# Kernel tuning notes

Measured on AMD Instinct MI355X. Metric: run time of the kernel, lower is better.

Reference implementation:

```python
import jax, jax.numpy as jnp
import numpy as np

SCALE = 20.0
THRESHOLD = 0.9995


def setup_inputs() -> dict:
    key = jax.random.key(0)
    k1, k2, k3 = jax.random.split(key, 3)
    B, C, H, W, S = 4, 128, 96, 128, 1024
    # L2-normalize along channel so the dot product is a true cosine in [-1, 1]
    # (keeps exp(scale * (x - threshold)) numerically sane, as intended by the module).
    def unit(x):
        return x / (jnp.linalg.norm(x, axis=1, keepdims=True) + 1e-8)
    source_feature_map = unit(jax.random.normal(k1, (B, C, H, W), dtype=jnp.float32))
    target_feature_map = unit(jax.random.normal(k2, (B, C, H, W), dtype=jnp.float32))
    source_feature_1D_locations = jax.random.randint(k3, (B, S, 1), 0, H * W, dtype=jnp.int64)
    mask = jnp.ones((B, 1, H, W), dtype=jnp.float32)
    return {
        "source_feature_map": source_feature_map,
        "target_feature_map": target_feature_map,
        "source_feature_1D_locations": source_feature_1D_locations,
        "mask": mask,
    }


def reference(source_feature_map, target_feature_map, source_feature_1D_locations, mask):
    B, C, H, W = source_feature_map.shape
    loc = source_feature_1D_locations[..., 0]  # [B, S]
    src_flat = source_feature_map.reshape(B, C, H * W)  # [B, C, HW]
    # gather sampled query vectors: [B, C, S]
    sampled = jnp.take_along_axis(src_flat, loc[:, None, :], axis=2)
    # per-batch 1x1 conv == batched matmul: [B, S, H, W]
    corr = jnp.einsum('bchw,bcs->bshw', target_feature_map, sampled)
    resp = jnp.exp(SCALE * (0.5 * corr + 0.5 - THRESHOLD)) * mask  # mask broadcasts [B,1,H,W]
    resp = resp / jnp.sum(resp, axis=(2, 3), keepdims=True)
    return resp
```

## Files before the change

kernel.cpp:

```cpp
#include <hip/hip_runtime.h>

typedef unsigned int u32;
typedef unsigned short u16;
typedef short s8v __attribute__((ext_vector_type(8)));
typedef float f16v __attribute__((ext_vector_type(16)));
typedef _Float16 h8 __attribute__((ext_vector_type(8)));

#define NB 4
#define NC 128
#define HW 12288
#define NS 1024

#define EXP_A 10.0f
#define EXP_B (-9.99f)
#define ESCALE 4096.0f

#define TS 256
#define TP 256
#define NPT (HW/TP)
#define NST (NS/TS)

__device__ inline u16 f2bf(float f) {
    u32 u = __float_as_uint(f);
    return (u16)((u + 0x7fffu + ((u >> 16) & 1u)) >> 16);
}
__device__ inline float bf2f(u16 h) { return __uint_as_float(((u32)h) << 16); }

__device__ inline void gload_lds16(const void* g, void* l) {
    __builtin_amdgcn_global_load_lds(
        (const __attribute__((address_space(1))) void*)g,
        (__attribute__((address_space(3))) void*)l, 16, 0, 0);
}

__global__ __launch_bounds__(256) void prep(
    const float* __restrict__ src, const float* __restrict__ tgt,
    const int* __restrict__ loc,
    u16* __restrict__ ahi, u16* __restrict__ alo,
    u16* __restrict__ bhi, u16* __restrict__ blo,
    float* __restrict__ sums)
{
    int blk = blockIdx.x, t = threadIdx.x;
    if (blk < (HW / 64) * NB) {
        int b = blk / (HW / 64), pt = blk - b * (HW / 64);
        int pxl = t & 63, u = t >> 6;
        int px = pt * 64 + pxl;
        int slot = u ^ ((px >> 1) & 3);
#pragma unroll
        for (int kc = 0; kc < 4; ++kc) {
            int c0 = kc * 32 + u * 8;
            u32 hq[4], lq[4];
#pragma unroll
            for (int k = 0; k < 4; ++k) {
                float v0 = tgt[((size_t)(b * NC + c0 + 2 * k)) * HW + px];
                float v1 = tgt[((size_t)(b * NC + c0 + 2 * k + 1)) * HW + px];
                u16 h0 = f2bf(v0), h1 = f2bf(v1);
                u16 l0 = f2bf(v0 - bf2f(h0)), l1 = f2bf(v1 - bf2f(h1));
                hq[k] = (u32)h0 | ((u32)h1 << 16);
                lq[k] = (u32)l0 | ((u32)l1 << 16);
            }
            size_t off = (((size_t)((b * 4 + kc) * HW + px)) * 4 + slot) * 8;
            *(uint4*)(bhi + off) = make_uint4(hq[0], hq[1], hq[2], hq[3]);
            *(uint4*)(blo + off) = make_uint4(lq[0], lq[1], lq[2], lq[3]);
        }
    } else {
        int sb = blk - (HW / 64) * NB;
        int gid = sb * 256 + t;
        if (gid < NB * NS) sums[gid] = 0.0f;
        int bs = sb * 2 + (t >> 7);
        int c  = t & 127;
        int b  = bs >> 10, s = bs & 1023;
        int l  = loc[bs];
        float v = src[((size_t)(b * NC + c)) * HW + l];
        u16 h  = f2bf(v);
        u16 lo = f2bf(v - bf2f(h));
        int kc = c >> 5, u = (c >> 3) & 3, e = c & 7;
        int slot = u ^ ((s >> 1) & 3);
        size_t off = ((size_t)((b * 4 + kc) * NS + s)) * 32 + slot * 8 + e;
        ahi[off] = h;
        alo[off] = lo;
    }
}

template <int F16>
__global__ __launch_bounds__(512) void corr_fused(
    const u16* __restrict__ bhi, const u16* __restrict__ blo,
    const u16* __restrict__ ahi, const u16* __restrict__ alo,
    const float* __restrict__ mask, float* __restrict__ sums,
    _Float16* __restrict__ ebuf, float* __restrict__ out)
{
    __shared__ __align__(1024) char sm[65536];

    int f = blockIdx.x;
    int xcd = f & 7, r0 = f >> 3;
    int st = r0 & 3;
    int p  = (r0 >> 2) * 8 + xcd;
    int b  = p / 48, pt = p - b * 48;

    int t = threadIdx.x, w = t >> 6, l = t & 63, ln = l & 31, h = l >> 5;
    int ws = w >> 1, wp = w & 1;

    f16v acc[2][4];
#pragma unroll
    for (int i = 0; i < 2; ++i)
#pragma unroll
        for (int j = 0; j < 4; ++j)
#pragma unroll
            for (int r = 0; r < 16; ++r) acc[i][j][r] = 0.0f;

    for (int kc = 0; kc < 4; ++kc) {
        const char* ga_h = (const char*)ahi + ((size_t)((b * 4 + kc) * NS + st * TS)) * 64;
        const char* ga_l = (const char*)alo + ((size_t)((b * 4 + kc) * NS + st * TS)) * 64;
        const char* gb_h = (const char*)bhi + ((size_t)((b * 4 + kc) * HW + pt * TP)) * 64;
        const char* gb_l = (const char*)blo + ((size_t)((b * 4 + kc) * HW + pt * TP)) * 64;
#pragma unroll
        for (int it = 0; it < 8; ++it) {
            int q = w * 8 + it;
            int rg = q >> 4, inner = q & 15;
            const char* gb = rg == 0 ? ga_h : rg == 1 ? ga_l : rg == 2 ? gb_h : gb_l;
            gload_lds16(gb + inner * 1024 + l * 16, sm + q * 1024);
        }
        __syncthreads();

#pragma unroll
        for (int kk2 = 0; kk2 < 2; ++kk2) {
            int u = kk2 * 2 + h;
            s8v a_h[2], a_l[2], b_h[4], b_l[4];
#pragma unroll
            for (int i = 0; i < 2; ++i) {
                int row = ws * 64 + i * 32 + ln;
                int sl = u ^ ((row >> 1) & 3);
                a_h[i] = *(const s8v*)(sm + 0 * 16384 + row * 64 + sl * 16);
                a_l[i] = *(const s8v*)(sm + 1 * 16384 + row * 64 + sl * 16);
            }
#pragma unroll
            for (int j = 0; j < 4; ++j) {
                int px = wp * 128 + j * 32 + ln;
                int sl = u ^ ((px >> 1) & 3);
                b_h[j] = *(const s8v*)(sm + 2 * 16384 + px * 64 + sl * 16);
                b_l[j] = *(const s8v*)(sm + 3 * 16384 + px * 64 + sl * 16);
            }
            __builtin_amdgcn_s_setprio(1);
#pragma unroll
            for (int i = 0; i < 2; ++i)
#pragma unroll
                for (int j = 0; j < 4; ++j) {
                    acc[i][j] = __builtin_amdgcn_mfma_f32_32x32x16_bf16(a_h[i], b_h[j], acc[i][j], 0, 0, 0);
                    acc[i][j] = __builtin_amdgcn_mfma_f32_32x32x16_bf16(a_l[i], b_h[j], acc[i][j], 0, 0, 0);
                    acc[i][j] = __builtin_amdgcn_mfma_f32_32x32x16_bf16(a_h[i], b_l[j], acc[i][j], 0, 0, 0);
                }
            __builtin_amdgcn_s_setprio(0);
        }
        __syncthreads();
    }

    float mvs[4];
#pragma unroll
    for (int j = 0; j < 4; ++j)
        mvs[j] = mask[(size_t)b * HW + pt * TP + wp * 128 + j * 32 + ln] * ESCALE;

    float* rs = (float*)sm;
    size_t base = ((size_t)(b * NS + st * TS)) * HW + pt * TP + wp * 128 + ln;
    _Float16* eb0 = ebuf + base;
    float*    ob0 = out  + base;
#pragma unroll
    for (int i = 0; i < 2; ++i) {
        int rb = ws * 64 + i * 32 + 4 * h;
#pragma unroll
        for (int r = 0; r < 16; ++r) {
            int row = rb + (r & 3) + 8 * (r >> 2);
            float tot = 0.0f;
#pragma unroll
            for (int j = 0; j < 4; ++j) {
                float e = __expf(fmaf(acc[i][j][r], EXP_A, EXP_B)) * mvs[j];
                if (F16) eb0[(size_t)row * HW + j * 32] = (_Float16)e;
                else     ob0[(size_t)row * HW + j * 32] = e;
                tot += e;
            }
            rs[(wp * TS + row) * 32 + ln] = tot;
        }
    }
    __syncthreads();
    int row2 = t & 255, half = t >> 8;
    float tot = 0.0f;
#pragma unroll
    for (int c = 0; c < 32; ++c)
        tot += rs[(half * TS + row2) * 32 + ((c + t) & 31)];
    atomicAdd(&sums[b * NS + st * TS + row2], tot);
}

__global__ __launch_bounds__(256) void rescale16(
    const float* __restrict__ sums, const _Float16* __restrict__ ebuf,
    float* __restrict__ out)
{
    int bs = blockIdx.x;
    float inv = 1.0f / sums[bs];
    const h8* p = (const h8*)(ebuf + (size_t)bs * HW);
    float4* o = (float4*)(out + (size_t)bs * HW);
    int t = threadIdx.x;
#pragma unroll
    for (int i = 0; i < 6; ++i) {
        int idx = t + i * 256;
        h8 v = p[idx];
        float4 a, c;
        a.x = (float)v[0] * inv; a.y = (float)v[1] * inv;
        a.z = (float)v[2] * inv; a.w = (float)v[3] * inv;
        c.x = (float)v[4] * inv; c.y = (float)v[5] * inv;
        c.z = (float)v[6] * inv; c.w = (float)v[7] * inv;
        o[2 * idx]     = a;
        o[2 * idx + 1] = c;
    }
}

__global__ __launch_bounds__(256) void rescale32(
    const float* __restrict__ sums, float* __restrict__ out)
{
    int bs = blockIdx.x;
    float inv = 1.0f / sums[bs];
    float4* p = (float4*)(out + (size_t)bs * HW);
    int t = threadIdx.x;
#pragma unroll
    for (int i = 0; i < 12; ++i) {
        float4 v = p[t + i * 256];
        v.x *= inv; v.y *= inv; v.z *= inv; v.w *= inv;
        p[t + i * 256] = v;
    }
}

extern "C" void kernel_launch(void* const* d_in, const int* in_sizes, int n_in,
                              void* d_out, int out_size, void* d_ws, size_t ws_size,
                              hipStream_t stream) {
    const float* src  = (const float*)d_in[0];
    const float* tgt  = (const float*)d_in[1];
    const int*   loc  = (const int*)d_in[2];
    const float* mask = (const float*)d_in[3];
    float* out = (float*)d_out;

    char* ws = (char*)d_ws;
    const size_t BPLANE = (size_t)NB * 4 * HW * 32 * sizeof(u16);
    const size_t APLANE = (size_t)NB * 4 * NS * 32 * sizeof(u16);
    const size_t EPLANE = (size_t)NB * NS * HW * sizeof(_Float16);
    u16* bhi = (u16*)ws;
    u16* blo = (u16*)(ws + BPLANE);
    u16* ahi = (u16*)(ws + 2 * BPLANE);
    u16* alo = (u16*)(ws + 2 * BPLANE + APLANE);
    float* sums = (float*)(ws + 2 * BPLANE + 2 * APLANE);
    _Float16* ebuf = (_Float16*)(ws + 2 * BPLANE + 2 * APLANE + 65536);
    const size_t NEED = 2 * BPLANE + 2 * APLANE + 65536 + EPLANE;

    prep<<<dim3((HW / 64) * NB + NB * NS / 2), 256, 0, stream>>>(
        src, tgt, loc, ahi, alo, bhi, blo, sums);

    dim3 g(NPT * NST * NB);
    if (ws_size >= NEED) {
        corr_fused<1><<<g, 512, 0, stream>>>(bhi, blo, ahi, alo, mask, sums, ebuf, out);
        rescale16<<<dim3(NB * NS), 256, 0, stream>>>(sums, ebuf, out);
    } else {
        corr_fused<0><<<g, 512, 0, stream>>>(bhi, blo, ahi, alo, mask, sums, ebuf, out);
        rescale32<<<dim3(NB * NS), 256, 0, stream>>>(sums, out);
    }
}
```

Measured before the change: 325.7 us.

## Halve sample tile to 128 rows with 256-thread blocks and XCD-aware grid mapping

The correlation kernel now uses 128-sample by 256-pixel tiles with 4 waves per block instead of 256x256 with 8 waves. LDS per block drops to 48KB and launch bounds request 2 blocks per CU. The block index is remapped so all row tiles for one pixel tile stay on the same XCD, which should improve L2 reuse of the B operand. The trade-off is that B is reloaded twice as often overall, in exchange for more blocks and better occupancy and latency hiding.

```diff
diff --git a/kernel.cpp b/kernel.cpp
--- a/kernel.cpp
+++ b/kernel.cpp
@@ -15,10 +15,10 @@
 #define EXP_B (-9.99f)
 #define ESCALE 4096.0f
 
-#define TS 256
+#define TSR 128
 #define TP 256
 #define NPT (HW/TP)
-#define NST (NS/TS)
+#define NRT ((NB*NS)/TSR)
 
 __device__ inline u16 f2bf(float f) {
     u32 u = __float_as_uint(f);
@@ -82,19 +82,19 @@
 }
 
 template <int F16>
-__global__ __launch_bounds__(512) void corr_fused(
+__global__ __launch_bounds__(256, 2) void corr_fused(
     const u16* __restrict__ bhi, const u16* __restrict__ blo,
     const u16* __restrict__ ahi, const u16* __restrict__ alo,
     const float* __restrict__ mask, float* __restrict__ sums,
     _Float16* __restrict__ ebuf, float* __restrict__ out)
 {
-    __shared__ __align__(1024) char sm[65536];
+    __shared__ __align__(1024) char sm[49152];
 
     int f = blockIdx.x;
-    int xcd = f & 7, r0 = f >> 3;
-    int st = r0 & 3;
-    int p  = (r0 >> 2) * 8 + xcd;
-    int b  = p / 48, pt = p - b * 48;
+    int xcd = f & 7, r = f >> 3;
+    int pt = xcd * 6 + (r >> 5);
+    int rt = r & 31;
+    int b  = rt >> 3, st2 = rt & 7;
 
     int t = threadIdx.x, w = t >> 6, l = t & 63, ln = l & 31, h = l >> 5;
     int ws = w >> 1, wp = w & 1;
@@ -105,19 +105,22 @@
 #pragma unroll
         for (int j = 0; j < 4; ++j)
 #pragma unroll
-            for (int r = 0; r < 16; ++r) acc[i][j][r] = 0.0f;
+            for (int r2 = 0; r2 < 16; ++r2) acc[i][j][r2] = 0.0f;
 
     for (int kc = 0; kc < 4; ++kc) {
-        const char* ga_h = (const char*)ahi + ((size_t)((b * 4 + kc) * NS + st * TS)) * 64;
-        const char* ga_l = (const char*)alo + ((size_t)((b * 4 + kc) * NS + st * TS)) * 64;
+        const char* ga_h = (const char*)ahi + ((size_t)((b * 4 + kc) * NS + st2 * TSR)) * 64;
+        const char* ga_l = (const char*)alo + ((size_t)((b * 4 + kc) * NS + st2 * TSR)) * 64;
         const char* gb_h = (const char*)bhi + ((size_t)((b * 4 + kc) * HW + pt * TP)) * 64;
         const char* gb_l = (const char*)blo + ((size_t)((b * 4 + kc) * HW + pt * TP)) * 64;
 #pragma unroll
-        for (int it = 0; it < 8; ++it) {
-            int q = w * 8 + it;
-            int rg = q >> 4, inner = q & 15;
-            const char* gb = rg == 0 ? ga_h : rg == 1 ? ga_l : rg == 2 ? gb_h : gb_l;
-            gload_lds16(gb + inner * 1024 + l * 16, sm + q * 1024);
+        for (int it = 0; it < 12; ++it) {
+            int q = w * 12 + it;
+            const char* g; int inner;
+            if (q < 8)       { g = ga_h; inner = q; }
+            else if (q < 16) { g = ga_l; inner = q - 8; }
+            else if (q < 32) { g = gb_h; inner = q - 16; }
+            else             { g = gb_l; inner = q - 32; }
+            gload_lds16(g + inner * 1024 + l * 16, sm + q * 1024);
         }
         __syncthreads();
 
@@ -129,15 +132,15 @@
             for (int i = 0; i < 2; ++i) {
                 int row = ws * 64 + i * 32 + ln;
                 int sl = u ^ ((row >> 1) & 3);
-                a_h[i] = *(const s8v*)(sm + 0 * 16384 + row * 64 + sl * 16);
-                a_l[i] = *(const s8v*)(sm + 1 * 16384 + row * 64 + sl * 16);
+                a_h[i] = *(const s8v*)(sm + 0 * 8192 + row * 64 + sl * 16);
+                a_l[i] = *(const s8v*)(sm + 1 * 8192 + row * 64 + sl * 16);
             }
 #pragma unroll
             for (int j = 0; j < 4; ++j) {
                 int px = wp * 128 + j * 32 + ln;
                 int sl = u ^ ((px >> 1) & 3);
-                b_h[j] = *(const s8v*)(sm + 2 * 16384 + px * 64 + sl * 16);
-                b_l[j] = *(const s8v*)(sm + 3 * 16384 + px * 64 + sl * 16);
+                b_h[j] = *(const s8v*)(sm + 16384 + px * 64 + sl * 16);
+                b_l[j] = *(const s8v*)(sm + 32768 + px * 64 + sl * 16);
             }
             __builtin_amdgcn_s_setprio(1);
 #pragma unroll
@@ -159,33 +162,33 @@
         mvs[j] = mask[(size_t)b * HW + pt * TP + wp * 128 + j * 32 + ln] * ESCALE;
 
     float* rs = (float*)sm;
-    size_t base = ((size_t)(b * NS + st * TS)) * HW + pt * TP + wp * 128 + ln;
+    size_t base = ((size_t)(b * NS + st2 * TSR)) * HW + pt * TP + wp * 128 + ln;
     _Float16* eb0 = ebuf + base;
     float*    ob0 = out  + base;
 #pragma unroll
     for (int i = 0; i < 2; ++i) {
         int rb = ws * 64 + i * 32 + 4 * h;
 #pragma unroll
-        for (int r = 0; r < 16; ++r) {
-            int row = rb + (r & 3) + 8 * (r >> 2);
+        for (int r2 = 0; r2 < 16; ++r2) {
+            int row = rb + (r2 & 3) + 8 * (r2 >> 2);
             float tot = 0.0f;
 #pragma unroll
             for (int j = 0; j < 4; ++j) {
-                float e = __expf(fmaf(acc[i][j][r], EXP_A, EXP_B)) * mvs[j];
+                float e = __expf(fmaf(acc[i][j][r2], EXP_A, EXP_B)) * mvs[j];
                 if (F16) eb0[(size_t)row * HW + j * 32] = (_Float16)e;
                 else     ob0[(size_t)row * HW + j * 32] = e;
                 tot += e;
             }
-            rs[(wp * TS + row) * 32 + ln] = tot;
+            rs[(wp * TSR + row) * 32 + ln] = tot;
         }
     }
     __syncthreads();
-    int row2 = t & 255, half = t >> 8;
+    int row2 = t & 127, half = t >> 7;
     float tot = 0.0f;
 #pragma unroll
     for (int c = 0; c < 32; ++c)
-        tot += rs[(half * TS + row2) * 32 + ((c + t) & 31)];
-    atomicAdd(&sums[b * NS + st * TS + row2], tot);
+        tot += rs[(half * TSR + row2) * 32 + ((c + t) & 31)];
+    atomicAdd(&sums[b * NS + st2 * TSR + row2], tot);
 }
 
 __global__ __launch_bounds__(256) void rescale16(
@@ -250,12 +253,12 @@
     prep<<<dim3((HW / 64) * NB + NB * NS / 2), 256, 0, stream>>>(
         src, tgt, loc, ahi, alo, bhi, blo, sums);
 
-    dim3 g(NPT * NST * NB);
+    dim3 g(NPT * NRT);
     if (ws_size >= NEED) {
-        corr_fused<1><<<g, 512, 0, stream>>>(bhi, blo, ahi, alo, mask, sums, ebuf, out);
+        corr_fused<1><<<g, 256, 0, stream>>>(bhi, blo, ahi, alo, mask, sums, ebuf, out);
         rescale16<<<dim3(NB * NS), 256, 0, stream>>>(sums, ebuf, out);
     } else {
-        corr_fused<0><<<g, 512, 0, stream>>>(bhi, blo, ahi, alo, mask, sums, ebuf, out);
+        corr_fused<0><<<g, 256, 0, stream>>>(bhi, blo, ahi, alo, mask, sums, ebuf, out);
         rescale32<<<dim3(NB * NS), 256, 0, stream>>>(sums, out);
     }
 }
```

New measurement: 327.8 us. About the same (+0.6%).

## Double-buffer LDS staging in corr_fused and remap blocks to keep pixel tiles per XCD

Applied to the files above, without the earlier changes.

Shared memory is doubled to two 64KB buffers so the global-to-LDS DMA for the next channel chunk is issued before the MFMA work on the current chunk, overlapping loads with compute. The block index decode changes so each XCD owns a contiguous range of pixel tiles and iterates over batch and sample tiles inside it, aiming for better L2 locality. The grid size is unchanged. The larger LDS footprint, 128KB per block, likely limits each CU to one resident block, which can lose latency hiding that two blocks per CU gave before. With only four K-chunks, the pipelining has little room to pay off.

```diff
diff --git a/kernel.cpp b/kernel.cpp
--- a/kernel.cpp
+++ b/kernel.cpp
@@ -18,7 +18,7 @@
 #define TS 256
 #define TP 256
 #define NPT (HW/TP)
-#define NST (NS/TS)
+#define NST ((NB*NS)/TS)
 
 __device__ inline u16 f2bf(float f) {
     u32 u = __float_as_uint(f);
@@ -88,13 +88,13 @@
     const float* __restrict__ mask, float* __restrict__ sums,
     _Float16* __restrict__ ebuf, float* __restrict__ out)
 {
-    __shared__ __align__(1024) char sm[65536];
+    __shared__ __align__(1024) char sm[131072];
 
     int f = blockIdx.x;
-    int xcd = f & 7, r0 = f >> 3;
-    int st = r0 & 3;
-    int p  = (r0 >> 2) * 8 + xcd;
-    int b  = p / 48, pt = p - b * 48;
+    int xcd = f & 7, r = f >> 3;
+    int pt  = xcd * 6 + (r >> 4);
+    int rt  = r & 15;
+    int b   = rt >> 2, st = rt & 3;
 
     int t = threadIdx.x, w = t >> 6, l = t & 63, ln = l & 31, h = l >> 5;
     int ws = w >> 1, wp = w & 1;
@@ -105,22 +105,30 @@
 #pragma unroll
         for (int j = 0; j < 4; ++j)
 #pragma unroll
-            for (int r = 0; r < 16; ++r) acc[i][j][r] = 0.0f;
-
-    for (int kc = 0; kc < 4; ++kc) {
+            for (int r2 = 0; r2 < 16; ++r2) acc[i][j][r2] = 0.0f;
+
+    auto STAGE = [&](int kc, int buf) {
         const char* ga_h = (const char*)ahi + ((size_t)((b * 4 + kc) * NS + st * TS)) * 64;
         const char* ga_l = (const char*)alo + ((size_t)((b * 4 + kc) * NS + st * TS)) * 64;
         const char* gb_h = (const char*)bhi + ((size_t)((b * 4 + kc) * HW + pt * TP)) * 64;
         const char* gb_l = (const char*)blo + ((size_t)((b * 4 + kc) * HW + pt * TP)) * 64;
+        char* dst = sm + buf * 65536;
 #pragma unroll
         for (int it = 0; it < 8; ++it) {
             int q = w * 8 + it;
             int rg = q >> 4, inner = q & 15;
-            const char* gb = rg == 0 ? ga_h : rg == 1 ? ga_l : rg == 2 ? gb_h : gb_l;
-            gload_lds16(gb + inner * 1024 + l * 16, sm + q * 1024);
-        }
-        __syncthreads();
-
+            const char* g = rg == 0 ? ga_h : rg == 1 ? ga_l : rg == 2 ? gb_h : gb_l;
+            gload_lds16(g + inner * 1024 + l * 16, dst + q * 1024);
+        }
+    };
+
+    STAGE(0, 0);
+    __syncthreads();
+
+    for (int kc = 0; kc < 4; ++kc) {
+        if (kc < 3) STAGE(kc + 1, (kc + 1) & 1);
+
+        const char* base = sm + (kc & 1) * 65536;
 #pragma unroll
         for (int kk2 = 0; kk2 < 2; ++kk2) {
             int u = kk2 * 2 + h;
@@ -129,15 +137,15 @@
             for (int i = 0; i < 2; ++i) {
                 int row = ws * 64 + i * 32 + ln;
                 int sl = u ^ ((row >> 1) & 3);
-                a_h[i] = *(const s8v*)(sm + 0 * 16384 + row * 64 + sl * 16);
-                a_l[i] = *(const s8v*)(sm + 1 * 16384 + row * 64 + sl * 16);
+                a_h[i] = *(const s8v*)(base + 0 * 16384 + row * 64 + sl * 16);
+                a_l[i] = *(const s8v*)(base + 1 * 16384 + row * 64 + sl * 16);
             }
 #pragma unroll
             for (int j = 0; j < 4; ++j) {
                 int px = wp * 128 + j * 32 + ln;
                 int sl = u ^ ((px >> 1) & 3);
-                b_h[j] = *(const s8v*)(sm + 2 * 16384 + px * 64 + sl * 16);
-                b_l[j] = *(const s8v*)(sm + 3 * 16384 + px * 64 + sl * 16);
+                b_h[j] = *(const s8v*)(base + 2 * 16384 + px * 64 + sl * 16);
+                b_l[j] = *(const s8v*)(base + 3 * 16384 + px * 64 + sl * 16);
             }
             __builtin_amdgcn_s_setprio(1);
 #pragma unroll
@@ -159,19 +167,19 @@
         mvs[j] = mask[(size_t)b * HW + pt * TP + wp * 128 + j * 32 + ln] * ESCALE;
 
     float* rs = (float*)sm;
-    size_t base = ((size_t)(b * NS + st * TS)) * HW + pt * TP + wp * 128 + ln;
-    _Float16* eb0 = ebuf + base;
-    float*    ob0 = out  + base;
+    size_t obase = ((size_t)(b * NS + st * TS)) * HW + pt * TP + wp * 128 + ln;
+    _Float16* eb0 = ebuf + obase;
+    float*    ob0 = out  + obase;
 #pragma unroll
     for (int i = 0; i < 2; ++i) {
         int rb = ws * 64 + i * 32 + 4 * h;
 #pragma unroll
-        for (int r = 0; r < 16; ++r) {
-            int row = rb + (r & 3) + 8 * (r >> 2);
+        for (int r2 = 0; r2 < 16; ++r2) {
+            int row = rb + (r2 & 3) + 8 * (r2 >> 2);
             float tot = 0.0f;
 #pragma unroll
             for (int j = 0; j < 4; ++j) {
-                float e = __expf(fmaf(acc[i][j][r], EXP_A, EXP_B)) * mvs[j];
+                float e = __expf(fmaf(acc[i][j][r2], EXP_A, EXP_B)) * mvs[j];
                 if (F16) eb0[(size_t)row * HW + j * 32] = (_Float16)e;
                 else     ob0[(size_t)row * HW + j * 32] = e;
                 tot += e;
@@ -250,7 +258,7 @@
     prep<<<dim3((HW / 64) * NB + NB * NS / 2), 256, 0, stream>>>(
         src, tgt, loc, ahi, alo, bhi, blo, sums);
 
-    dim3 g(NPT * NST * NB);
+    dim3 g(NPT * NST);
     if (ws_size >= NEED) {
         corr_fused<1><<<g, 512, 0, stream>>>(bhi, blo, ahi, alo, mask, sums, ebuf, out);
         rescale16<<<dim3(NB * NS), 256, 0, stream>>>(sums, ebuf, out);
```

Measured after the change: 326.6 us. Within noise of the previous version (+0.3%).
